# Kernel optimization log

Hardware: AMD Instinct MI355X
Metric: run time of the kernel (lower is better)

Reference implementation:

```python
import jax, jax.numpy as jnp
import numpy as np

PATCH = 128
FEATHER = 4  # config.fusion_feather_size
EPS = 1e-8


def _gaussian2d(f):
    k = 2 * f + 1
    sigma = f / 3.0
    x = jnp.arange(k, dtype=jnp.float32) - f
    g = jnp.exp(-0.5 * (x / sigma) ** 2)
    g = g / g.sum()
    return g[:, None] * g[None, :]


def setup_inputs() -> dict:
    key = jax.random.key(0)
    k1, k2, k3, k4, k5 = jax.random.split(key, 5)
    H, W, N = 2160, 3840, 256
    original_image = jax.random.normal(k1, (1, 3, H, W), jnp.float32)
    repaired_patches = jax.random.normal(k2, (N, 3, PATCH, PATCH), jnp.float32)
    holes_mask = (jax.random.uniform(k3, (1, 1, H, W)) < 0.05).astype(jnp.float32)
    pos_y = jax.random.randint(k4, (N,), 0, H - PATCH, jnp.int32)
    pos_x = jax.random.randint(k5, (N,), 0, W - PATCH, jnp.int32)
    return {"original_image": original_image, "repaired_patches": repaired_patches,
            "holes_mask": holes_mask, "pos_y": pos_y, "pos_x": pos_x}


def _feather_masks(holes_mask, pos_y, pos_x):
    # gather per-patch hole regions [N,P,P] (positions are constants -> parallel gather)
    m = holes_mask[0, 0]
    gather = jax.vmap(lambda y, x: jax.lax.dynamic_slice(m, (y, x), (PATCH, PATCH)))
    holes = gather(pos_y, pos_x)  # [N,P,P]
    kern = _gaussian2d(FEATHER)[None, None]  # [1,1,9,9]
    fm = jax.lax.conv_general_dilated(
        holes[:, None], kern, (1, 1), [(FEATHER, FEATHER), (FEATHER, FEATHER)])
    return fm[:, 0]  # [N,P,P]


def _masked_stats(img, nh):
    # per-channel masked mean/std over H,W (nh broadcasts over channels)
    denom = jnp.sum(nh, axis=(2, 3), keepdims=True)
    mean = jnp.sum(img * nh, axis=(2, 3), keepdims=True) / denom
    std = jnp.sqrt(jnp.sum((img - mean) ** 2 * nh, axis=(2, 3), keepdims=True) / denom)
    return mean, std


def reference(original_image, repaired_patches, holes_mask, pos_y, pos_x):
    fm = _feather_masks(holes_mask, pos_y, pos_x)  # [N,P,P]
    result0 = original_image[0]  # [3,H,W]

    # sequential scatter: each patch blends against the current result (patches may overlap)
    def step(res, inp):
        patch, f, y, x = inp
        region = jax.lax.dynamic_slice(res, (0, y, x), (3, PATCH, PATCH))
        fused = region * (1.0 - f[None]) + patch * f[None]
        return jax.lax.dynamic_update_slice(res, fused, (0, y, x)), None

    result, _ = jax.lax.scan(step, result0, (repaired_patches, fm, pos_y, pos_x))
    fused_image = result[None]  # [1,3,H,W]

    # color correction: match hole-region stats to original non-hole stats
    nh = 1.0 - holes_mask
    om, os = _masked_stats(original_image, nh)
    fmn, fs = _masked_stats(fused_image, nh)
    hole_region = fused_image * holes_mask
    corrected_hole = (hole_region - fmn) * (os / (fs + EPS)) + om
    corrected = fused_image * (1.0 - holes_mask) + corrected_hole * holes_mask
    return corrected
```

## Files before the change

### kernel.cpp

```cpp
#include <hip/hip_runtime.h>

#define HH 2160
#define WW 3840
#define NPATCH 256
#define PSZ 128
#define HW_ (HH*WW)
#define FMSZ (NPATCH*PSZ*PSZ)

#define TW 256
#define TH 8
#define NBX (WW/TW)
#define NBY (HH/TH)
#define NB  (NBX*NBY)

typedef float fx4 __attribute__((ext_vector_type(4)));

#define COEF_OFF  ((size_t)FMSZ*4)
#define PART_OFF  (COEF_OFF + 64)

__global__ __launch_bounds__(256) void feather_kernel(
        const float* __restrict__ mask, const int* __restrict__ pos_y,
        const int* __restrict__ pos_x, float* __restrict__ fm) {
    __shared__ float sm[40*PSZ];
    __shared__ float tp[40*PSZ];
    const int n = blockIdx.x;
    const int r0 = blockIdx.y * 32;
    const int y0 = pos_y[n], x0 = pos_x[n];
    float g[9]; float s = 0.f;
    #pragma unroll
    for (int k = 0; k < 9; ++k) { float xx = (k-4)*0.75f; g[k] = expf(-0.5f*xx*xx); s += g[k]; }
    const float inv = 1.f/s;
    #pragma unroll
    for (int k = 0; k < 9; ++k) g[k] *= inv;

    for (int idx = threadIdx.x; idx < 40*PSZ; idx += 256) {
        int l = idx >> 7, j = idx & 127;
        int r = r0 + l - 4;
        sm[idx] = ((unsigned)r < (unsigned)PSZ) ? mask[(y0+r)*WW + (x0+j)] : 0.f;
    }
    __syncthreads();
    for (int idx = threadIdx.x; idx < 40*PSZ; idx += 256) {
        int l = idx >> 7, j = idx & 127;
        float a = 0.f;
        #pragma unroll
        for (int d = -4; d <= 4; ++d) {
            int jj = j + d;
            if (jj >= 0 && jj < PSZ) a += sm[(l<<7)+jj]*g[d+4];
        }
        tp[idx] = a;
    }
    __syncthreads();
    float* o = fm + n*(PSZ*PSZ) + r0*PSZ;
    for (int idx = threadIdx.x; idx < 32*PSZ; idx += 256) {
        int i = idx >> 7, j = idx & 127;
        float a = 0.f;
        #pragma unroll
        for (int d = 0; d < 9; ++d) a += tp[((i+d)<<7)+j]*g[d];
        o[idx] = a;
    }
}

__global__ __launch_bounds__(512) void compose_kernel(
        const float* __restrict__ orig, const float* __restrict__ patches,
        const float* __restrict__ mask, const int* __restrict__ pos_y,
        const int* __restrict__ pos_x, const float* __restrict__ fm,
        float* __restrict__ out, float* __restrict__ partial) {
    __shared__ int ln[NPATCH];
    __shared__ int ly[NPATCH];
    __shared__ int lx[NPATCH];
    __shared__ unsigned long long wm[4];
    __shared__ float red[8][13];

    const int tid = threadIdx.x;
    const int lane = tid & 63;
    const int wid  = tid >> 6;
    const int tx0 = blockIdx.x * TW;
    const int ty0 = blockIdx.y * TH;

    if (tid < NPATCH) {
        const int yn = pos_y[tid], xn = pos_x[tid];
        const bool cov = (yn < ty0 + TH) && (yn + PSZ > ty0) &&
                         (xn < tx0 + TW) && (xn + PSZ > tx0);
        unsigned long long b = __ballot(cov);
        if (lane == 0) wm[wid] = b;
        __syncthreads();
        if (cov) {
            int pos = __popcll(b & ((1ull << lane) - 1ull));
            for (int w = 0; w < wid; ++w) pos += __popcll(wm[w]);
            ln[pos] = tid; ly[pos] = yn; lx[pos] = xn;
        }
    } else {
        __syncthreads();
    }
    __syncthreads();
    const int cnt = __popcll(wm[0]) + __popcll(wm[1]) + __popcll(wm[2]) + __popcll(wm[3]);

    const int x0 = tx0 + lane * 4;
    const int y  = ty0 + wid;

    const fx4* __restrict__ mask4 = (const fx4*)mask;
    const fx4* __restrict__ orig4 = (const fx4*)orig;
    fx4* __restrict__ out4 = (fx4*)out;

    const int q = (y*WW + x0) >> 2;
    const fx4 m = mask4[q];
    fx4 v0 = __builtin_nontemporal_load(&orig4[q]);
    fx4 v1 = __builtin_nontemporal_load(&orig4[(HW_ >> 2) + q]);
    fx4 v2 = __builtin_nontemporal_load(&orig4[((2*HW_) >> 2) + q]);

    const float nhx = 1.f-m.x, nhy = 1.f-m.y, nhz = 1.f-m.z, nhw = 1.f-m.w;
    const float a_cnt = nhx+nhy+nhz+nhw;
    const float so1x = v0.x*nhx+v0.y*nhy+v0.z*nhz+v0.w*nhw;
    const float so2x = v0.x*v0.x*nhx+v0.y*v0.y*nhy+v0.z*v0.z*nhz+v0.w*v0.w*nhw;
    const float so1y = v1.x*nhx+v1.y*nhy+v1.z*nhz+v1.w*nhw;
    const float so2y = v1.x*v1.x*nhx+v1.y*v1.y*nhy+v1.z*v1.z*nhz+v1.w*v1.w*nhw;
    const float so1z = v2.x*nhx+v2.y*nhy+v2.z*nhz+v2.w*nhw;
    const float so2z = v2.x*v2.x*nhx+v2.y*v2.y*nhy+v2.z*v2.z*nhz+v2.w*v2.w*nhw;

    for (int k = 0; k < cnt; ++k) {
        const int dy = y - ly[k];
        if ((unsigned)dy >= (unsigned)PSZ) continue;
        const int dx0 = x0 - lx[k];
        if (dx0 <= -4 || dx0 >= PSZ) continue;
        const int nn = ln[k];
        const int rowb = dy << 7;
        const float* __restrict__ fmp = fm + nn*(PSZ*PSZ) + rowb;
        const float* __restrict__ pp  = patches + nn*(3*PSZ*PSZ) + rowb;
        #define BLEND(J, MX) { \
            const int dx = dx0 + J; \
            if ((unsigned)dx < (unsigned)PSZ) { \
                const float f = fmp[dx]; const float of = 1.f - f; \
                v0.MX = v0.MX*of + pp[dx]*f; \
                v1.MX = v1.MX*of + pp[dx + PSZ*PSZ]*f; \
                v2.MX = v2.MX*of + pp[dx + 2*PSZ*PSZ]*f; \
            } }
        BLEND(0, x) BLEND(1, y) BLEND(2, z) BLEND(3, w)
        #undef BLEND
    }

    out4[q] = v0;
    out4[(HW_ >> 2) + q] = v1;
    out4[((2*HW_) >> 2) + q] = v2;

    const float sf1x = v0.x*nhx+v0.y*nhy+v0.z*nhz+v0.w*nhw;
    const float sf2x = v0.x*v0.x*nhx+v0.y*v0.y*nhy+v0.z*v0.z*nhz+v0.w*v0.w*nhw;
    const float sf1y = v1.x*nhx+v1.y*nhy+v1.z*nhz+v1.w*nhw;
    const float sf2y = v1.x*v1.x*nhx+v1.y*v1.y*nhy+v1.z*v1.z*nhz+v1.w*v1.w*nhw;
    const float sf1z = v2.x*nhx+v2.y*nhy+v2.z*nhz+v2.w*nhw;
    const float sf2z = v2.x*v2.x*nhx+v2.y*v2.y*nhy+v2.z*v2.z*nhz+v2.w*v2.w*nhw;

    float vals[13] = {a_cnt, so1x,so1y,so1z, so2x,so2y,so2z,
                      sf1x,sf1y,sf1z, sf2x,sf2y,sf2z};
    #pragma unroll
    for (int v = 0; v < 13; ++v) {
        float t = vals[v];
        t += __shfl_down(t, 32); t += __shfl_down(t, 16);
        t += __shfl_down(t, 8);  t += __shfl_down(t, 4);
        t += __shfl_down(t, 2);  t += __shfl_down(t, 1);
        if (lane == 0) red[wid][v] = t;
    }
    __syncthreads();
    if (tid < 13) {
        const int bid = blockIdx.y * NBX + blockIdx.x;
        float sgl = 0.f;
        #pragma unroll
        for (int w = 0; w < 8; ++w) sgl += red[w][tid];
        partial[tid*NB + bid] = sgl;
    }
}

__global__ __launch_bounds__(832) void finalize_kernel(
        const float* __restrict__ partial, float* __restrict__ coef) {
    __shared__ double tot[13];
    const int w = threadIdx.x >> 6;
    const int lane = threadIdx.x & 63;
    const float* p = partial + w*NB;
    double s0 = 0.0, s1 = 0.0;
    int b = lane;
    for (; b + 64 < NB; b += 128) { s0 += (double)p[b]; s1 += (double)p[b+64]; }
    if (b < NB) s0 += (double)p[b];
    double t = s0 + s1;
    t += __shfl_down(t, 32); t += __shfl_down(t, 16);
    t += __shfl_down(t, 8);  t += __shfl_down(t, 4);
    t += __shfl_down(t, 2);  t += __shfl_down(t, 1);
    if (lane == 0) tot[w] = t;
    __syncthreads();
    if (threadIdx.x == 0) {
        const double cnt = tot[0];
        for (int c = 0; c < 3; ++c) {
            double om = tot[1+c]/cnt;
            double ov = tot[4+c]/cnt - om*om;
            double os = sqrt(ov > 0.0 ? ov : 0.0);
            double fmn = tot[7+c]/cnt;
            double fv = tot[10+c]/cnt - fmn*fmn;
            double fs = sqrt(fv > 0.0 ? fv : 0.0);
            coef[c]   = (float)(os/(fs + 1e-8));
            coef[3+c] = (float)fmn;
            coef[6+c] = (float)om;
        }
    }
}

__global__ __launch_bounds__(256) void correct_kernel(
        float* __restrict__ out, const float* __restrict__ mask,
        const float* __restrict__ coef) {
    const int q = blockIdx.x * 256 + threadIdx.x;
    if (q >= (HW_ >> 2)) return;
    const fx4 m = ((const fx4*)mask)[q];
    if (m.x == 0.f && m.y == 0.f && m.z == 0.f && m.w == 0.f) return;
    const float r0 = coef[0], r1 = coef[1], r2 = coef[2];
    const float f0 = coef[3], f1 = coef[4], f2 = coef[5];
    const float o0 = coef[6], o1 = coef[7], o2 = coef[8];
    fx4* __restrict__ out4 = (fx4*)out;
    fx4 v0 = out4[q];
    fx4 v1 = out4[(HW_>>2)+q];
    fx4 v2 = out4[((2*HW_)>>2)+q];
    if (m.x != 0.f) { v0.x=(v0.x-f0)*r0+o0; v1.x=(v1.x-f1)*r1+o1; v2.x=(v2.x-f2)*r2+o2; }
    if (m.y != 0.f) { v0.y=(v0.y-f0)*r0+o0; v1.y=(v1.y-f1)*r1+o1; v2.y=(v2.y-f2)*r2+o2; }
    if (m.z != 0.f) { v0.z=(v0.z-f0)*r0+o0; v1.z=(v1.z-f1)*r1+o1; v2.z=(v2.z-f2)*r2+o2; }
    if (m.w != 0.f) { v0.w=(v0.w-f0)*r0+o0; v1.w=(v1.w-f1)*r1+o1; v2.w=(v2.w-f2)*r2+o2; }
    out4[q] = v0;
    out4[(HW_>>2)+q] = v1;
    out4[((2*HW_)>>2)+q] = v2;
}

extern "C" void kernel_launch(void* const* d_in, const int* in_sizes, int n_in,
                              void* d_out, int out_size, void* d_ws, size_t ws_size,
                              hipStream_t stream) {
    const float* orig    = (const float*)d_in[0];
    const float* patches = (const float*)d_in[1];
    const float* mask    = (const float*)d_in[2];
    const int*   pos_y   = (const int*)d_in[3];
    const int*   pos_x   = (const int*)d_in[4];
    float* out = (float*)d_out;

    float* fm      = (float*)d_ws;
    float* coef    = (float*)((char*)d_ws + COEF_OFF);
    float* partial = (float*)((char*)d_ws + PART_OFF);

    dim3 fg(NPATCH, 4);
    feather_kernel<<<fg, 256, 0, stream>>>(mask, pos_y, pos_x, fm);
    dim3 g(NBX, NBY);
    compose_kernel<<<g, 512, 0, stream>>>(orig, patches, mask, pos_y, pos_x, fm,
                                          out, partial);
    finalize_kernel<<<1, 832, 0, stream>>>(partial, coef);
    correct_kernel<<<((HW_ >> 2) + 255)/256, 256, 0, stream>>>(out, mask, coef);
}
```

Measured before the change: 138.2 us.

## Split compose across channels and pack hole mask into bytes for correction

The compose kernel now launches a third grid dimension with one channel per block. Each thread processes a single channel, which cuts register pressure and triples the number of blocks, but the mask, patch-list build and feather-mask reads are repeated once per channel. The block reduction is restructured to produce per-channel partial statistics. Compose also writes a compact byte-per-quad hole bitmap, so the correction kernel reads 1 byte instead of 16 per quad and skips hole-free regions cheaply. If the workspace is too small, the old full-mask correction path is used.

```diff
diff --git a/kernel.cpp b/kernel.cpp
--- a/kernel.cpp
+++ b/kernel.cpp
@@ -14,9 +14,12 @@
 #define NB  (NBX*NBY)
 
 typedef float fx4 __attribute__((ext_vector_type(4)));
+typedef unsigned char uchar;
 
 #define COEF_OFF  ((size_t)FMSZ*4)
 #define PART_OFF  (COEF_OFF + 64)
+#define HBB_OFF   ((PART_OFF + (size_t)13*NB*4 + 63)/64*64)
+#define WS_NEED   (HBB_OFF + (size_t)(HW_/4))
 
 __global__ __launch_bounds__(256) void feather_kernel(
         const float* __restrict__ mask, const int* __restrict__ pos_y,
@@ -64,18 +67,20 @@
         const float* __restrict__ orig, const float* __restrict__ patches,
         const float* __restrict__ mask, const int* __restrict__ pos_y,
         const int* __restrict__ pos_x, const float* __restrict__ fm,
-        float* __restrict__ out, float* __restrict__ partial) {
+        float* __restrict__ out, float* __restrict__ partial,
+        uchar* __restrict__ hbb) {
     __shared__ int ln[NPATCH];
     __shared__ int ly[NPATCH];
     __shared__ int lx[NPATCH];
     __shared__ unsigned long long wm[4];
-    __shared__ float red[8][13];
+    __shared__ float sv[5][520];
 
     const int tid = threadIdx.x;
     const int lane = tid & 63;
     const int wid  = tid >> 6;
     const int tx0 = blockIdx.x * TW;
     const int ty0 = blockIdx.y * TH;
+    const int chan = blockIdx.z;
 
     if (tid < NPATCH) {
         const int yn = pos_y[tid], xn = pos_x[tid];
@@ -103,19 +108,14 @@
     fx4* __restrict__ out4 = (fx4*)out;
 
     const int q = (y*WW + x0) >> 2;
+    const int pq = chan*(HW_ >> 2) + q;
     const fx4 m = mask4[q];
-    fx4 v0 = __builtin_nontemporal_load(&orig4[q]);
-    fx4 v1 = __builtin_nontemporal_load(&orig4[(HW_ >> 2) + q]);
-    fx4 v2 = __builtin_nontemporal_load(&orig4[((2*HW_) >> 2) + q]);
+    fx4 v = __builtin_nontemporal_load(&orig4[pq]);
 
     const float nhx = 1.f-m.x, nhy = 1.f-m.y, nhz = 1.f-m.z, nhw = 1.f-m.w;
     const float a_cnt = nhx+nhy+nhz+nhw;
-    const float so1x = v0.x*nhx+v0.y*nhy+v0.z*nhz+v0.w*nhw;
-    const float so2x = v0.x*v0.x*nhx+v0.y*v0.y*nhy+v0.z*v0.z*nhz+v0.w*v0.w*nhw;
-    const float so1y = v1.x*nhx+v1.y*nhy+v1.z*nhz+v1.w*nhw;
-    const float so2y = v1.x*v1.x*nhx+v1.y*v1.y*nhy+v1.z*v1.z*nhz+v1.w*v1.w*nhw;
-    const float so1z = v2.x*nhx+v2.y*nhy+v2.z*nhz+v2.w*nhw;
-    const float so2z = v2.x*v2.x*nhx+v2.y*v2.y*nhy+v2.z*v2.z*nhz+v2.w*v2.w*nhw;
+    const float s1o = v.x*nhx+v.y*nhy+v.z*nhz+v.w*nhw;
+    const float s2o = v.x*v.x*nhx+v.y*v.y*nhy+v.z*v.z*nhz+v.w*v.w*nhw;
 
     for (int k = 0; k < cnt; ++k) {
         const int dy = y - ly[k];
@@ -125,47 +125,42 @@
         const int nn = ln[k];
         const int rowb = dy << 7;
         const float* __restrict__ fmp = fm + nn*(PSZ*PSZ) + rowb;
-        const float* __restrict__ pp  = patches + nn*(3*PSZ*PSZ) + rowb;
+        const float* __restrict__ pp  = patches + (nn*3 + chan)*(PSZ*PSZ) + rowb;
         #define BLEND(J, MX) { \
             const int dx = dx0 + J; \
             if ((unsigned)dx < (unsigned)PSZ) { \
-                const float f = fmp[dx]; const float of = 1.f - f; \
-                v0.MX = v0.MX*of + pp[dx]*f; \
-                v1.MX = v1.MX*of + pp[dx + PSZ*PSZ]*f; \
-                v2.MX = v2.MX*of + pp[dx + 2*PSZ*PSZ]*f; \
+                const float f = fmp[dx]; \
+                v.MX = v.MX*(1.f - f) + pp[dx]*f; \
             } }
         BLEND(0, x) BLEND(1, y) BLEND(2, z) BLEND(3, w)
         #undef BLEND
     }
 
-    out4[q] = v0;
-    out4[(HW_ >> 2) + q] = v1;
-    out4[((2*HW_) >> 2) + q] = v2;
-
-    const float sf1x = v0.x*nhx+v0.y*nhy+v0.z*nhz+v0.w*nhw;
-    const float sf2x = v0.x*v0.x*nhx+v0.y*v0.y*nhy+v0.z*v0.z*nhz+v0.w*v0.w*nhw;
-    const float sf1y = v1.x*nhx+v1.y*nhy+v1.z*nhz+v1.w*nhw;
-    const float sf2y = v1.x*v1.x*nhx+v1.y*v1.y*nhy+v1.z*v1.z*nhz+v1.w*v1.w*nhw;
-    const float sf1z = v2.x*nhx+v2.y*nhy+v2.z*nhz+v2.w*nhw;
-    const float sf2z = v2.x*v2.x*nhx+v2.y*v2.y*nhy+v2.z*v2.z*nhz+v2.w*v2.w*nhw;
-
-    float vals[13] = {a_cnt, so1x,so1y,so1z, so2x,so2y,so2z,
-                      sf1x,sf1y,sf1z, sf2x,sf2y,sf2z};
-    #pragma unroll
-    for (int v = 0; v < 13; ++v) {
-        float t = vals[v];
+    out4[pq] = v;
+
+    const float s1f = v.x*nhx+v.y*nhy+v.z*nhz+v.w*nhw;
+    const float s2f = v.x*v.x*nhx+v.y*v.y*nhy+v.z*v.z*nhz+v.w*v.w*nhw;
+
+    if (chan == 0 && hbb) {
+        const unsigned hb = (unsigned)(m.x!=0.f) | ((unsigned)(m.y!=0.f)<<1)
+                          | ((unsigned)(m.z!=0.f)<<2) | ((unsigned)(m.w!=0.f)<<3);
+        hbb[q] = (uchar)hb;
+    }
+
+    sv[0][tid] = s1o; sv[1][tid] = s2o; sv[2][tid] = s1f; sv[3][tid] = s2f; sv[4][tid] = a_cnt;
+    __syncthreads();
+    if (wid < 5 && !(wid == 4 && chan != 0)) {
+        const float* p = sv[wid];
+        float t = p[lane] + p[lane+64] + p[lane+128] + p[lane+192]
+                + p[lane+256] + p[lane+320] + p[lane+384] + p[lane+448];
         t += __shfl_down(t, 32); t += __shfl_down(t, 16);
         t += __shfl_down(t, 8);  t += __shfl_down(t, 4);
         t += __shfl_down(t, 2);  t += __shfl_down(t, 1);
-        if (lane == 0) red[wid][v] = t;
-    }
-    __syncthreads();
-    if (tid < 13) {
-        const int bid = blockIdx.y * NBX + blockIdx.x;
-        float sgl = 0.f;
-        #pragma unroll
-        for (int w = 0; w < 8; ++w) sgl += red[w][tid];
-        partial[tid*NB + bid] = sgl;
+        if (lane == 0) {
+            const int bid = blockIdx.y * NBX + blockIdx.x;
+            const int stat = (wid == 4) ? 0 : (1 + 3*wid + chan);
+            partial[stat*NB + bid] = t;
+        }
     }
 }
 
@@ -202,6 +197,35 @@
 }
 
 __global__ __launch_bounds__(256) void correct_kernel(
+        float* __restrict__ out, const unsigned int* __restrict__ hbb4,
+        const float* __restrict__ coef) {
+    const int i = blockIdx.x * 256 + threadIdx.x;
+    if (i >= (HW_ >> 4)) return;
+    const unsigned h4 = hbb4[i];
+    if (h4 == 0u) return;
+    const float r0 = coef[0], r1 = coef[1], r2 = coef[2];
+    const float f0 = coef[3], f1 = coef[4], f2 = coef[5];
+    const float o0 = coef[6], o1 = coef[7], o2 = coef[8];
+    fx4* __restrict__ out4 = (fx4*)out;
+    #pragma unroll
+    for (int b = 0; b < 4; ++b) {
+        const unsigned bits = (h4 >> (8*b)) & 15u;
+        if (!bits) continue;
+        const int q = i*4 + b;
+        fx4 v0 = out4[q];
+        fx4 v1 = out4[(HW_>>2)+q];
+        fx4 v2 = out4[((2*HW_)>>2)+q];
+        if (bits & 1u) { v0.x=(v0.x-f0)*r0+o0; v1.x=(v1.x-f1)*r1+o1; v2.x=(v2.x-f2)*r2+o2; }
+        if (bits & 2u) { v0.y=(v0.y-f0)*r0+o0; v1.y=(v1.y-f1)*r1+o1; v2.y=(v2.y-f2)*r2+o2; }
+        if (bits & 4u) { v0.z=(v0.z-f0)*r0+o0; v1.z=(v1.z-f1)*r1+o1; v2.z=(v2.z-f2)*r2+o2; }
+        if (bits & 8u) { v0.w=(v0.w-f0)*r0+o0; v1.w=(v1.w-f1)*r1+o1; v2.w=(v2.w-f2)*r2+o2; }
+        out4[q] = v0;
+        out4[(HW_>>2)+q] = v1;
+        out4[((2*HW_)>>2)+q] = v2;
+    }
+}
+
+__global__ __launch_bounds__(256) void correct_full_kernel(
         float* __restrict__ out, const float* __restrict__ mask,
         const float* __restrict__ coef) {
     const int q = blockIdx.x * 256 + threadIdx.x;
@@ -237,12 +261,20 @@
     float* fm      = (float*)d_ws;
     float* coef    = (float*)((char*)d_ws + COEF_OFF);
     float* partial = (float*)((char*)d_ws + PART_OFF);
+    uchar* hbb     = (uchar*)((char*)d_ws + HBB_OFF);
+
+    const bool use_hbb = (ws_size >= WS_NEED);
 
     dim3 fg(NPATCH, 4);
     feather_kernel<<<fg, 256, 0, stream>>>(mask, pos_y, pos_x, fm);
-    dim3 g(NBX, NBY);
+    dim3 g(NBX, NBY, 3);
     compose_kernel<<<g, 512, 0, stream>>>(orig, patches, mask, pos_y, pos_x, fm,
-                                          out, partial);
+                                          out, partial, use_hbb ? hbb : nullptr);
     finalize_kernel<<<1, 832, 0, stream>>>(partial, coef);
-    correct_kernel<<<((HW_ >> 2) + 255)/256, 256, 0, stream>>>(out, mask, coef);
-}
+    if (use_hbb) {
+        correct_kernel<<<((HW_ >> 4) + 255)/256, 256, 0, stream>>>(
+            out, (const unsigned int*)hbb, coef);
+    } else {
+        correct_full_kernel<<<((HW_ >> 2) + 255)/256, 256, 0, stream>>>(out, mask, coef);
+    }
+}
```

After: 143.5 us. 1.04x slower.
